# Kernel optimization log

Measured on AMD Instinct MI355X. Metric: run time of the kernel, lower is better.

Reference implementation:

```python
import jax, jax.numpy as jnp
import numpy as np
import math

DIMS, K_SIZE, V_SIZE = 1024, 128, 128

def setup_inputs() -> dict:
    key = jax.random.key(0)
    ks = jax.random.split(key, 7)
    B, S = 4, 2048
    scale = 1.0 / math.sqrt(DIMS)
    return {
        "inputs": jax.random.normal(ks[0], (B, S, DIMS), dtype=jnp.float32),
        "Wq": jax.random.normal(ks[1], (DIMS, K_SIZE), dtype=jnp.float32) * scale,
        "bq": jnp.zeros((K_SIZE,), dtype=jnp.float32),
        "Wk": jax.random.normal(ks[2], (DIMS, K_SIZE), dtype=jnp.float32) * scale,
        "bk": jnp.zeros((K_SIZE,), dtype=jnp.float32),
        "Wv": jax.random.normal(ks[3], (DIMS, V_SIZE), dtype=jnp.float32) * scale,
        "bv": jnp.zeros((V_SIZE,), dtype=jnp.float32),
    }

def reference(inputs, Wq, bq, Wk, bk, Wv, bv):
    # inputs: [B, S, D]
    q = inputs @ Wq + bq            # [B, S, k]
    k = inputs @ Wk + bk            # [B, S, k]
    v = inputs @ Wv + bv            # [B, S, v]
    logits = jnp.einsum('bqk,bsk->bqs', q, k)  # [B, S, S]
    S = inputs.shape[1]
    causal = jnp.tril(jnp.ones((S, S), dtype=bool))  # allow j <= i (triu k=1 masked)
    logits = jnp.where(causal, logits, -jnp.inf)
    probs = jax.nn.softmax(logits / jnp.sqrt(jnp.float32(Wk.shape[1])), axis=-1)
    read = jnp.einsum('bqs,bsv->bqv', probs, v)  # [B, S, v]
    return jnp.concatenate([inputs, read], axis=-1)  # [B, S, D+v]
```

## Files before the change

### kernel.cpp

```cpp
#include <hip/hip_runtime.h>
#include <hip/hip_bf16.h>

typedef __attribute__((ext_vector_type(8))) short bf16x8;
typedef __attribute__((ext_vector_type(4))) float f32x4;
typedef __attribute__((ext_vector_type(8))) unsigned short u16x8;
typedef __attribute__((ext_vector_type(4))) float float4_t;

static constexpr int Bn = 4, Sn = 2048, Dn = 1024, Kn = 128;
static constexpr int ODn = Dn + Kn;
static constexpr int CH = 4;
static constexpr int CPB = 144;
static constexpr float L2E = 1.4426950408889634f;

__device__ __forceinline__ unsigned short f2bf(float f) {
    union { float f; unsigned int u; } v; v.f = f;
    unsigned int u = v.u;
    return (unsigned short)((u + 0x7fffu + ((u >> 16) & 1u)) >> 16);
}
__device__ __forceinline__ float bf2f(unsigned short h) {
    union { float f; unsigned int u; } v; v.u = ((unsigned int)h) << 16;
    return v.f;
}

#define GLOAD16(g, l) __builtin_amdgcn_global_load_lds( \
    (const __attribute__((address_space(1))) void*)(g), \
    (__attribute__((address_space(3))) void*)(l), 16, 0, 0)

__global__ __launch_bounds__(256) void wt_prep(const float* __restrict__ Wq,
                                               const float* __restrict__ Wk,
                                               const float* __restrict__ Wv,
                                               unsigned short* __restrict__ Wt) {
    __shared__ unsigned short tile[32][34];
    int k0 = blockIdx.x * 32, c0 = blockIdx.y * 32, w = blockIdx.z;
    const float* W = (w == 0) ? Wq : (w == 1) ? Wk : Wv;
    int tc = threadIdx.x & 31;
    int tr = (threadIdx.x >> 5) * 4;
#pragma unroll
    for (int i = 0; i < 4; ++i)
        tile[tr + i][tc] = f2bf(W[(size_t)(k0 + tr + i) * Kn + c0 + tc]);
    __syncthreads();
    unsigned short* dst = Wt + (size_t)w * Kn * Dn;
#pragma unroll
    for (int i = 0; i < 4; ++i)
        dst[(size_t)(c0 + tr + i) * Dn + k0 + tc] = tile[tc][tr + i];
}

__global__ __launch_bounds__(256, 2) void proj_kernel(
    const float* __restrict__ X, const unsigned short* __restrict__ Wt,
    const float* __restrict__ bq, const float* __restrict__ bk, const float* __restrict__ bv,
    float* __restrict__ out,
    unsigned short* __restrict__ qws, unsigned short* __restrict__ kws,
    unsigned short* __restrict__ vtws) {
    __shared__ __align__(16) unsigned short Alds[2][64 * 64];
    __shared__ __align__(16) unsigned short Wlds[2][96 * 64];
    const int orig = blockIdx.x;
    const int wg = (orig & 7) * 64 + (orig >> 3);
    const int m0 = (wg >> 2) * 64;
    const int ns = wg & 3;
    const int c0 = ns * 96;
    const int t = threadIdx.x, lane = t & 63, wn = t >> 6;
    const int lr = lane & 15, lg = lane >> 4;
    const int ar0 = t >> 3, ach = t & 7;

    const unsigned short* wsrcp[3]; int wdst[3];
#pragma unroll
    for (int p = 0; p < 3; ++p) {
        int s = t + p * 256, col = s >> 3, kseg = s & 7;
        wsrcp[p] = Wt + (size_t)(c0 + col) * Dn + ((kseg ^ (col & 7)) * 8);
        wdst[p] = col * 128 + kseg * 16;
    }
    const float* xbase = X + (size_t)(m0 + ar0) * Dn + ach * 8;
    float* obase = out + (size_t)(m0 + ar0) * ODn + ach * 8;
    f32x4 acc[6] = {};
    float4_t va[4];

    auto loadA = [&](int k0) {
        va[0] = *(const float4_t*)(xbase + k0);
        va[1] = *(const float4_t*)(xbase + k0 + 4);
        va[2] = *(const float4_t*)(xbase + (size_t)32 * Dn + k0);
        va[3] = *(const float4_t*)(xbase + (size_t)32 * Dn + k0 + 4);
    };
    auto stageW = [&](int buf, int k0) {
#pragma unroll
        for (int p = 0; p < 3; ++p)
            GLOAD16(wsrcp[p] + k0, (char*)&Wlds[buf][0] + wdst[p]);
    };
    auto writeA = [&](int buf, int k0) {
        if ((k0 >> 8) == ns) {
            *(float4_t*)(obase + k0) = va[0];
            *(float4_t*)(obase + k0 + 4) = va[1];
            *(float4_t*)(obase + (size_t)32 * ODn + k0) = va[2];
            *(float4_t*)(obase + (size_t)32 * ODn + k0 + 4) = va[3];
        }
        u16x8 h0, h1;
#pragma unroll
        for (int j = 0; j < 4; ++j) {
            h0[j] = f2bf(va[0][j]); h0[j + 4] = f2bf(va[1][j]);
            h1[j] = f2bf(va[2][j]); h1[j + 4] = f2bf(va[3][j]);
        }
        const int r1 = ar0 + 32;
        *(u16x8*)((char*)&Alds[buf][0] + ar0 * 128 + ((ach * 16) ^ ((ar0 & 7) << 4))) = h0;
        *(u16x8*)((char*)&Alds[buf][0] + r1 * 128 + ((ach * 16) ^ ((r1 & 7) << 4))) = h1;
    };

    loadA(0); stageW(0, 0); writeA(0, 0);
    __syncthreads();

    const int arow = wn * 16 + lr;
    const int asw = (arow & 7) << 4;
    for (int k0 = 0; k0 < Dn; k0 += 64) {
        const int cur = (k0 >> 6) & 1;
        const int kn = k0 + 64;
        if (kn < Dn) { loadA(kn); stageW(cur ^ 1, kn); }
        __builtin_amdgcn_s_setprio(1);
#pragma unroll
        for (int kk = 0; kk < 2; ++kk) {
            bf16x8 afr = *(const bf16x8*)((const char*)&Alds[cur][0] +
                          arow * 128 + ((kk * 64 + lg * 16) ^ asw));
#pragma unroll
            for (int ni = 0; ni < 6; ++ni) {
                int col = ni * 16 + lr;
                bf16x8 bfr = *(const bf16x8*)((const char*)&Wlds[cur][0] +
                              col * 128 + ((kk * 64 + lg * 16) ^ ((col & 7) << 4)));
                acc[ni] = __builtin_amdgcn_mfma_f32_16x16x32_bf16(afr, bfr, acc[ni], 0, 0, 0);
            }
        }
        __builtin_amdgcn_s_setprio(0);
        if (kn < Dn) writeA(cur ^ 1, kn);
        __syncthreads();
    }
#pragma unroll
    for (int ni = 0; ni < 6; ++ni) {
        int gcol = c0 + ni * 16 + lr;
        int buf = gcol >> 7, ci = gcol & 127;
        float bias = (buf == 0 ? bq : buf == 1 ? bk : bv)[ci];
#pragma unroll
        for (int r = 0; r < 4; ++r) {
            int grow = m0 + wn * 16 + lg * 4 + r;
            unsigned short hv = f2bf(acc[ni][r] + bias);
            if (buf == 0) qws[(size_t)grow * Kn + ci] = hv;
            else if (buf == 1) kws[(size_t)grow * Kn + ci] = hv;
            else {
                int bb = grow >> 11, ss = grow & 2047;
                vtws[((size_t)bb * Kn + ci) * Sn + ss] = hv;
            }
        }
    }
}

__global__ __launch_bounds__(256, 2) void attn_kernel(
    const unsigned short* __restrict__ qws, const unsigned short* __restrict__ kws,
    const unsigned short* __restrict__ vtws,
    unsigned short* __restrict__ part_o, float* __restrict__ part_ml) {
    __shared__ __align__(16) unsigned short Klds[2][64 * 128];
    __shared__ __align__(16) unsigned short Vlds[2][128 * 64];
    __shared__ __align__(16) unsigned short Plds[4][16 * 64];
    constexpr float SCALE = 0.08838834764831845f;
    const int t = threadIdx.x, lane = t & 63, wid = t >> 6;
    const int lr = lane & 15, lg = lane >> 4;
    const int pidx = blockIdx.x;
    const int b = pidx / CPB;
    const int idx = pidx - b * CPB;
    int qt = 0, rem = idx;
    while (true) { int n = (qt + CH) >> 2; if (rem < n) break; rem -= n; ++qt; }
    const int c = rem;
    const int it0 = c * CH;
    const int it1 = (it0 + CH < qt + 1) ? (it0 + CH) : (qt + 1);
    const int qrow0 = qt * 64 + wid * 16;

    const unsigned short* kb  = kws  + (size_t)b * Sn * Kn;
    const unsigned short* vtb = vtws + (size_t)b * Kn * Sn;
    const unsigned short* ksrc[4];
    const unsigned short* vsrc[4];
#pragma unroll
    for (int p = 0; p < 4; ++p) {
        int row = wid * 16 + p * 4 + (lane >> 4);
        int seg = lane & 15;
        ksrc[p] = kb + (size_t)row * Kn + ((seg ^ (row & 7)) * 8);
        int cc = wid * 32 + p * 8 + (lane >> 3);
        int sg = lane & 7;
        vsrc[p] = vtb + (size_t)cc * Sn + ((sg ^ (cc & 7)) * 8);
    }
    auto stage = [&](int buf, int it) {
#pragma unroll
        for (int p = 0; p < 4; ++p) {
            GLOAD16(ksrc[p] + (size_t)it * (64 * Kn), (char*)&Klds[buf][0] + wid * 4096 + p * 1024);
            GLOAD16(vsrc[p] + (size_t)it * 64,        (char*)&Vlds[buf][0] + wid * 4096 + p * 1024);
        }
    };

    const unsigned short* qbase = qws + ((size_t)b * Sn + qrow0) * Kn;
    bf16x8 qf[4];
#pragma unroll
    for (int kk = 0; kk < 4; ++kk)
        qf[kk] = *(const bf16x8*)(qbase + (size_t)lr * Kn + kk * 32 + lg * 8);
    f32x4 o[8] = {};
    float mrow[4] = {-1e30f, -1e30f, -1e30f, -1e30f};
    float lrow[4] = {0.f, 0.f, 0.f, 0.f};

    stage(0, it0);
    __syncthreads();

    for (int it = it0; it < it1; ++it) {
        const int cur = (it - it0) & 1;
        if (it + 1 < it1) stage(cur ^ 1, it + 1);
        const int kv0 = it * 64;
        f32x4 s[4] = {};
        __builtin_amdgcn_s_setprio(1);
#pragma unroll
        for (int n = 0; n < 4; ++n) {
            int kvr = n * 16 + lr;
#pragma unroll
            for (int kk = 0; kk < 4; ++kk) {
                int off = (kvr * 256 + kk * 64 + lg * 16) ^ ((kvr & 7) << 4);
                bf16x8 kf = *(const bf16x8*)((const char*)&Klds[cur][0] + off);
                s[n] = __builtin_amdgcn_mfma_f32_16x16x32_bf16(qf[kk], kf, s[n], 0, 0, 0);
            }
        }
        __builtin_amdgcn_s_setprio(0);
        if (it == qt) {
#pragma unroll
            for (int n = 0; n < 4; ++n) {
                int kvg = kv0 + n * 16 + lr;
#pragma unroll
                for (int r = 0; r < 4; ++r) {
                    float sv = s[n][r] * SCALE;
                    int qg = qrow0 + lg * 4 + r;
                    s[n][r] = (kvg > qg) ? -1e30f : sv;
                }
            }
        } else {
#pragma unroll
            for (int n = 0; n < 4; ++n)
#pragma unroll
                for (int r = 0; r < 4; ++r)
                    s[n][r] *= SCALE;
        }
        float tmax[4], rsum[4], alpha[4];
#pragma unroll
        for (int r = 0; r < 4; ++r)
            tmax[r] = fmaxf(fmaxf(s[0][r], s[1][r]), fmaxf(s[2][r], s[3][r]));
#pragma unroll
        for (int d = 1; d < 16; d <<= 1)
#pragma unroll
            for (int r = 0; r < 4; ++r)
                tmax[r] = fmaxf(tmax[r], __shfl_xor(tmax[r], d));
#pragma unroll
        for (int r = 0; r < 4; ++r) {
            float mnew = fmaxf(mrow[r], tmax[r]);
            alpha[r] = exp2f((mrow[r] - mnew) * L2E);
            mrow[r] = mnew;
            rsum[r] = 0.f;
        }
        unsigned short pb[4][4];
#pragma unroll
        for (int n = 0; n < 4; ++n)
#pragma unroll
            for (int r = 0; r < 4; ++r) {
                float p = exp2f((s[n][r] - mrow[r]) * L2E);
                rsum[r] += p;
                pb[n][r] = f2bf(p);
            }
#pragma unroll
        for (int d = 1; d < 16; d <<= 1)
#pragma unroll
            for (int r = 0; r < 4; ++r)
                rsum[r] += __shfl_xor(rsum[r], d);
#pragma unroll
        for (int r = 0; r < 4; ++r)
            lrow[r] = lrow[r] * alpha[r] + rsum[r];
#pragma unroll
        for (int v = 0; v < 8; ++v)
#pragma unroll
            for (int r = 0; r < 4; ++r)
                o[v][r] *= alpha[r];
        char* pbase = (char*)&Plds[wid][0];
#pragma unroll
        for (int n = 0; n < 4; ++n)
#pragma unroll
            for (int r = 0; r < 4; ++r) {
                int q = lg * 4 + r, kv = n * 16 + lr;
                int off = (q * 128 + kv * 2) ^ ((q & 7) << 4);
                *(unsigned short*)(pbase + off) = pb[n][r];
            }
        bf16x8 pa[2];
#pragma unroll
        for (int kk = 0; kk < 2; ++kk) {
            int aoff = (lr * 128 + kk * 64 + lg * 16) ^ ((lr & 7) << 4);
            pa[kk] = *(const bf16x8*)((const char*)pbase + aoff);
        }
        __builtin_amdgcn_s_setprio(1);
#pragma unroll
        for (int v = 0; v < 8; ++v) {
            int vcol = v * 16 + lr;
#pragma unroll
            for (int kk = 0; kk < 2; ++kk) {
                int boff = (vcol * 128 + kk * 64 + lg * 16) ^ ((vcol & 7) << 4);
                bf16x8 vb = *(const bf16x8*)((const char*)&Vlds[cur][0] + boff);
                o[v] = __builtin_amdgcn_mfma_f32_16x16x32_bf16(pa[kk], vb, o[v], 0, 0, 0);
            }
        }
        __builtin_amdgcn_s_setprio(0);
        __syncthreads();
    }
    const size_t pbo = (size_t)pidx * (64 * 128);
#pragma unroll
    for (int v = 0; v < 8; ++v)
#pragma unroll
        for (int r = 0; r < 4; ++r) {
            int row = wid * 16 + lg * 4 + r;
            part_o[pbo + (size_t)row * 128 + v * 16 + lr] = f2bf(o[v][r]);
        }
    if (lr == 0) {
#pragma unroll
        for (int r = 0; r < 4; ++r) {
            int row = wid * 16 + lg * 4 + r;
            part_ml[(size_t)pidx * 128 + row * 2]     = mrow[r];
            part_ml[(size_t)pidx * 128 + row * 2 + 1] = lrow[r];
        }
    }
}

__global__ __launch_bounds__(256) void reduce_kernel(
    const unsigned short* __restrict__ part_o, const float* __restrict__ part_ml,
    float* __restrict__ out) {
    const int bid = blockIdx.x;
    const int rh = bid & 1, bq = bid >> 1;
    const int qt = bq & 31, b = bq >> 5;
    const int nch = (qt + CH) >> 2;
    int idx0 = 0;
    for (int q = 0; q < qt; ++q) idx0 += (q + CH) >> 2;
    const int pidx0 = b * CPB + idx0;
    const int t = threadIdx.x;
    const int row = rh * 32 + (t >> 3);
    const int col0 = (t & 7) * 16;

    float mc[8], lc[8];
#pragma unroll
    for (int cc = 0; cc < 8; ++cc) { mc[cc] = -1e30f; lc[cc] = 0.f; }
#pragma unroll
    for (int cc = 0; cc < 8; ++cc)
        if (cc < nch) {
            mc[cc] = part_ml[(size_t)(pidx0 + cc) * 128 + row * 2];
            lc[cc] = part_ml[(size_t)(pidx0 + cc) * 128 + row * 2 + 1];
        }
    float m = -1e30f;
#pragma unroll
    for (int cc = 0; cc < 8; ++cc) m = fmaxf(m, mc[cc]);
    float l = 0.f;
    float accv[16] = {};
#pragma unroll
    for (int cc = 0; cc < 8; ++cc)
        if (cc < nch) {
            float w = exp2f((mc[cc] - m) * L2E);
            l += w * lc[cc];
            const unsigned short* po = part_o + (size_t)(pidx0 + cc) * (64 * 128) + (size_t)row * 128 + col0;
            bf16x8 v0 = *(const bf16x8*)(po);
            bf16x8 v1 = *(const bf16x8*)(po + 8);
#pragma unroll
            for (int j = 0; j < 8; ++j) {
                accv[j]     += w * bf2f((unsigned short)v0[j]);
                accv[8 + j] += w * bf2f((unsigned short)v1[j]);
            }
        }
    const float inv = 1.f / l;
    float* op = out + ((size_t)b * Sn + qt * 64 + row) * ODn + Dn + col0;
#pragma unroll
    for (int j = 0; j < 4; ++j) {
        float4_t v = { accv[j*4] * inv, accv[j*4+1] * inv, accv[j*4+2] * inv, accv[j*4+3] * inv };
        *(float4_t*)(op + j * 4) = v;
    }
}

extern "C" void kernel_launch(void* const* d_in, const int* in_sizes, int n_in,
                              void* d_out, int out_size, void* d_ws, size_t ws_size,
                              hipStream_t stream) {
    const float* X  = (const float*)d_in[0];
    const float* Wq = (const float*)d_in[1];
    const float* bq = (const float*)d_in[2];
    const float* Wk = (const float*)d_in[3];
    const float* bk = (const float*)d_in[4];
    const float* Wv = (const float*)d_in[5];
    const float* bv = (const float*)d_in[6];
    float* out = (float*)d_out;

    unsigned short* Wt   = (unsigned short*)d_ws;
    unsigned short* qws  = Wt  + (size_t)3 * Kn * Dn;
    unsigned short* kws  = qws + (size_t)Bn * Sn * Kn;
    unsigned short* vtws = kws + (size_t)Bn * Sn * Kn;
    unsigned short* part_o = vtws + (size_t)Bn * Sn * Kn;
    float* part_ml = (float*)(part_o + (size_t)Bn * CPB * 64 * 128);

    wt_prep<<<dim3(32, 4, 3), 256, 0, stream>>>(Wq, Wk, Wv, Wt);
    proj_kernel<<<512, 256, 0, stream>>>(X, Wt, bq, bk, bv, out, qws, kws, vtws);
    attn_kernel<<<Bn * CPB, 256, 0, stream>>>(qws, kws, vtws, part_o, part_ml);
    reduce_kernel<<<256, 256, 0, stream>>>(part_o, part_ml, out);
}
```

Before: 68.52 us.

## Triple-buffer projection GEMM with 2x2 warp tiling and lazy softmax rescale

The projection kernel moves to a triple-buffered W staging scheme with two register A buffers, explicit vmcnt waits and raw s_barrier, so global loads overlap MFMA work across more stages. Its warp tiling changes from 4x1 to 2x2 (32 rows x 48 cols per wave), which reuses each A and B fragment across more MFMAs. The attention kernel skips the running-max update and the rescale of the output accumulator when every row's new max exceeds the old one by at most 8, which removes exp and multiply work in most iterations. In exchange the skip can let probabilities reach about e^8 before rescaling, which costs some bf16 precision, and the hand-counted vmcnt values are fragile if the number of loads changes.

```diff
diff --git a/kernel.cpp b/kernel.cpp
--- a/kernel.cpp
+++ b/kernel.cpp
@@ -52,7 +52,8 @@
     unsigned short* __restrict__ qws, unsigned short* __restrict__ kws,
     unsigned short* __restrict__ vtws) {
     __shared__ __align__(16) unsigned short Alds[2][64 * 64];
-    __shared__ __align__(16) unsigned short Wlds[2][96 * 64];
+    __shared__ __align__(16) unsigned short Wlds[3][96 * 64];
+    constexpr int NT = 16;
     const int orig = blockIdx.x;
     const int wg = (orig & 7) * 64 + (orig >> 3);
     const int m0 = (wg >> 2) * 64;
@@ -60,6 +61,7 @@
     const int c0 = ns * 96;
     const int t = threadIdx.x, lane = t & 63, wn = t >> 6;
     const int lr = lane & 15, lg = lane >> 4;
+    const int wr = wn >> 1, wc = wn & 1;
     const int ar0 = t >> 3, ach = t & 7;
 
     const unsigned short* wsrcp[3]; int wdst[3];
@@ -71,22 +73,24 @@
     }
     const float* xbase = X + (size_t)(m0 + ar0) * Dn + ach * 8;
     float* obase = out + (size_t)(m0 + ar0) * ODn + ach * 8;
-    f32x4 acc[6] = {};
-    float4_t va[4];
-
-    auto loadA = [&](int k0) {
+    f32x4 acc[2][3] = {};
+    float4_t va0[4], va1[4];
+
+    auto loadA = [&](float4_t* va, int j) {
+        const int k0 = j * 64;
         va[0] = *(const float4_t*)(xbase + k0);
         va[1] = *(const float4_t*)(xbase + k0 + 4);
         va[2] = *(const float4_t*)(xbase + (size_t)32 * Dn + k0);
         va[3] = *(const float4_t*)(xbase + (size_t)32 * Dn + k0 + 4);
     };
-    auto stageW = [&](int buf, int k0) {
+    auto stageW = [&](int wbuf, int j) {
 #pragma unroll
         for (int p = 0; p < 3; ++p)
-            GLOAD16(wsrcp[p] + k0, (char*)&Wlds[buf][0] + wdst[p]);
+            GLOAD16(wsrcp[p] + j * 64, (char*)&Wlds[wbuf][0] + wdst[p]);
     };
-    auto writeA = [&](int buf, int k0) {
-        if ((k0 >> 8) == ns) {
+    auto writeA = [&](const float4_t* va, int abuf, int j) {
+        const int k0 = j * 64;
+        if ((j >> 2) == ns) {
             *(float4_t*)(obase + k0) = va[0];
             *(float4_t*)(obase + k0 + 4) = va[1];
             *(float4_t*)(obase + (size_t)32 * ODn + k0) = va[2];
@@ -94,55 +98,89 @@
         }
         u16x8 h0, h1;
 #pragma unroll
-        for (int j = 0; j < 4; ++j) {
-            h0[j] = f2bf(va[0][j]); h0[j + 4] = f2bf(va[1][j]);
-            h1[j] = f2bf(va[2][j]); h1[j + 4] = f2bf(va[3][j]);
+        for (int jj = 0; jj < 4; ++jj) {
+            h0[jj] = f2bf(va[0][jj]); h0[jj + 4] = f2bf(va[1][jj]);
+            h1[jj] = f2bf(va[2][jj]); h1[jj + 4] = f2bf(va[3][jj]);
         }
         const int r1 = ar0 + 32;
-        *(u16x8*)((char*)&Alds[buf][0] + ar0 * 128 + ((ach * 16) ^ ((ar0 & 7) << 4))) = h0;
-        *(u16x8*)((char*)&Alds[buf][0] + r1 * 128 + ((ach * 16) ^ ((r1 & 7) << 4))) = h1;
+        *(u16x8*)((char*)&Alds[abuf][0] + ar0 * 128 + ((ach * 16) ^ ((ar0 & 7) << 4))) = h0;
+        *(u16x8*)((char*)&Alds[abuf][0] + r1 * 128 + ((ach * 16) ^ ((r1 & 7) << 4))) = h1;
     };
-
-    loadA(0); stageW(0, 0); writeA(0, 0);
-    __syncthreads();
-
-    const int arow = wn * 16 + lr;
-    const int asw = (arow & 7) << 4;
-    for (int k0 = 0; k0 < Dn; k0 += 64) {
-        const int cur = (k0 >> 6) & 1;
-        const int kn = k0 + 64;
-        if (kn < Dn) { loadA(kn); stageW(cur ^ 1, kn); }
+    auto compute = [&](int abuf, int wbuf) {
         __builtin_amdgcn_s_setprio(1);
 #pragma unroll
         for (int kk = 0; kk < 2; ++kk) {
-            bf16x8 afr = *(const bf16x8*)((const char*)&Alds[cur][0] +
-                          arow * 128 + ((kk * 64 + lg * 16) ^ asw));
-#pragma unroll
-            for (int ni = 0; ni < 6; ++ni) {
-                int col = ni * 16 + lr;
-                bf16x8 bfr = *(const bf16x8*)((const char*)&Wlds[cur][0] +
-                              col * 128 + ((kk * 64 + lg * 16) ^ ((col & 7) << 4)));
-                acc[ni] = __builtin_amdgcn_mfma_f32_16x16x32_bf16(afr, bfr, acc[ni], 0, 0, 0);
-            }
+            bf16x8 afr[2], bfr[3];
+#pragma unroll
+            for (int mi = 0; mi < 2; ++mi) {
+                int row = wr * 32 + mi * 16 + lr;
+                afr[mi] = *(const bf16x8*)((const char*)&Alds[abuf][0] +
+                           row * 128 + ((kk * 64 + lg * 16) ^ ((row & 7) << 4)));
+            }
+#pragma unroll
+            for (int ni = 0; ni < 3; ++ni) {
+                int col = wc * 48 + ni * 16 + lr;
+                bfr[ni] = *(const bf16x8*)((const char*)&Wlds[wbuf][0] +
+                           col * 128 + ((kk * 64 + lg * 16) ^ ((col & 7) << 4)));
+            }
+#pragma unroll
+            for (int mi = 0; mi < 2; ++mi)
+#pragma unroll
+                for (int ni = 0; ni < 3; ++ni)
+                    acc[mi][ni] = __builtin_amdgcn_mfma_f32_16x16x32_bf16(afr[mi], bfr[ni], acc[mi][ni], 0, 0, 0);
         }
         __builtin_amdgcn_s_setprio(0);
-        if (kn < Dn) writeA(cur ^ 1, kn);
-        __syncthreads();
-    }
-#pragma unroll
-    for (int ni = 0; ni < 6; ++ni) {
-        int gcol = c0 + ni * 16 + lr;
+    };
+
+    loadA(va0, 0);  stageW(0, 0);
+    loadA(va1, 1);  stageW(1, 1);
+    writeA(va0, 0, 0);
+    asm volatile("s_waitcnt vmcnt(7) lgkmcnt(0)" ::: "memory");
+    __builtin_amdgcn_sched_barrier(0);
+    __builtin_amdgcn_s_barrier();
+    __builtin_amdgcn_sched_barrier(0);
+
+    for (int ii = 0; ii < 14; ii += 2) {
+        loadA(va0, ii + 2);  stageW((ii + 2) % 3, ii + 2);
+        compute(0, ii % 3);
+        writeA(va1, 1, ii + 1);
+        asm volatile("s_waitcnt vmcnt(7) lgkmcnt(0)" ::: "memory");
+        __builtin_amdgcn_sched_barrier(0);
+        __builtin_amdgcn_s_barrier();
+        __builtin_amdgcn_sched_barrier(0);
+        loadA(va1, ii + 3);  stageW((ii + 3) % 3, ii + 3);
+        compute(1, (ii + 1) % 3);
+        writeA(va0, 0, ii + 2);
+        asm volatile("s_waitcnt vmcnt(7) lgkmcnt(0)" ::: "memory");
+        __builtin_amdgcn_sched_barrier(0);
+        __builtin_amdgcn_s_barrier();
+        __builtin_amdgcn_sched_barrier(0);
+    }
+    compute(0, 14 % 3);
+    writeA(va1, 1, 15);
+    asm volatile("s_waitcnt vmcnt(0) lgkmcnt(0)" ::: "memory");
+    __builtin_amdgcn_sched_barrier(0);
+    __builtin_amdgcn_s_barrier();
+    __builtin_amdgcn_sched_barrier(0);
+    compute(1, 15 % 3);
+
+#pragma unroll
+    for (int ni = 0; ni < 3; ++ni) {
+        int gcol = c0 + wc * 48 + ni * 16 + lr;
         int buf = gcol >> 7, ci = gcol & 127;
         float bias = (buf == 0 ? bq : buf == 1 ? bk : bv)[ci];
 #pragma unroll
-        for (int r = 0; r < 4; ++r) {
-            int grow = m0 + wn * 16 + lg * 4 + r;
-            unsigned short hv = f2bf(acc[ni][r] + bias);
-            if (buf == 0) qws[(size_t)grow * Kn + ci] = hv;
-            else if (buf == 1) kws[(size_t)grow * Kn + ci] = hv;
-            else {
-                int bb = grow >> 11, ss = grow & 2047;
-                vtws[((size_t)bb * Kn + ci) * Sn + ss] = hv;
+        for (int mi = 0; mi < 2; ++mi) {
+#pragma unroll
+            for (int r = 0; r < 4; ++r) {
+                int grow = m0 + wr * 32 + mi * 16 + lg * 4 + r;
+                unsigned short hv = f2bf(acc[mi][ni][r] + bias);
+                if (buf == 0) qws[(size_t)grow * Kn + ci] = hv;
+                else if (buf == 1) kws[(size_t)grow * Kn + ci] = hv;
+                else {
+                    int bb = grow >> 11, ss = grow & 2047;
+                    vtws[((size_t)bb * Kn + ci) * Sn + ss] = hv;
+                }
             }
         }
     }
@@ -236,7 +274,7 @@
                 for (int r = 0; r < 4; ++r)
                     s[n][r] *= SCALE;
         }
-        float tmax[4], rsum[4], alpha[4];
+        float tmax[4], rsum[4];
 #pragma unroll
         for (int r = 0; r < 4; ++r)
             tmax[r] = fmaxf(fmaxf(s[0][r], s[1][r]), fmaxf(s[2][r], s[3][r]));
@@ -245,14 +283,23 @@
 #pragma unroll
             for (int r = 0; r < 4; ++r)
                 tmax[r] = fmaxf(tmax[r], __shfl_xor(tmax[r], d));
-#pragma unroll
-        for (int r = 0; r < 4; ++r) {
-            float mnew = fmaxf(mrow[r], tmax[r]);
-            alpha[r] = exp2f((mrow[r] - mnew) * L2E);
-            mrow[r] = mnew;
-            rsum[r] = 0.f;
+        float need = fmaxf(fmaxf(tmax[0] - mrow[0], tmax[1] - mrow[1]),
+                           fmaxf(tmax[2] - mrow[2], tmax[3] - mrow[3]));
+        if (!__all(need <= 8.0f)) {
+#pragma unroll
+            for (int r = 0; r < 4; ++r) {
+                float mnew = fmaxf(mrow[r], tmax[r]);
+                float alpha = exp2f((mrow[r] - mnew) * L2E);
+                mrow[r] = mnew;
+                lrow[r] *= alpha;
+#pragma unroll
+                for (int v = 0; v < 8; ++v)
+                    o[v][r] *= alpha;
+            }
         }
         unsigned short pb[4][4];
+#pragma unroll
+        for (int r = 0; r < 4; ++r) rsum[r] = 0.f;
 #pragma unroll
         for (int n = 0; n < 4; ++n)
 #pragma unroll
@@ -268,12 +315,7 @@
                 rsum[r] += __shfl_xor(rsum[r], d);
 #pragma unroll
         for (int r = 0; r < 4; ++r)
-            lrow[r] = lrow[r] * alpha[r] + rsum[r];
-#pragma unroll
-        for (int v = 0; v < 8; ++v)
-#pragma unroll
-            for (int r = 0; r < 4; ++r)
-                o[v][r] *= alpha[r];
+            lrow[r] += rsum[r];
         char* pbase = (char*)&Plds[wid][0];
 #pragma unroll
         for (int n = 0; n < 4; ++n)
```

New measurement: 66.85 us. 1.03x faster.
